# Kernel tuning notes

Hardware: AMD Instinct MI355X
Metric: run time of the kernel (lower is better)

The kernel has to match this reference:

```python
import jax, jax.numpy as jnp
import numpy as np

B, N, IN, OUT = 16, 1000, 128, 128


def setup_inputs() -> dict:
    key = jax.random.key(0)
    ks = jax.random.split(key, 8)
    stdv = 1.0 / np.sqrt(IN + OUT)  # matches reset_param uniform(-stdv, stdv)
    def w(k):
        return jax.random.uniform(k, (N, IN + OUT, OUT), jnp.float32, -stdv, stdv)
    return {
        "xt": jax.random.normal(ks[0], (B, N, IN), jnp.float32),
        "hidden": jax.random.normal(ks[1], (1, N, OUT), jnp.float32),
        "ct_1": jax.random.normal(ks[2], (1, N, OUT), jnp.float32),
        "W_i": w(ks[3]), "b_i": jnp.zeros((N, OUT), jnp.float32),
        "W_o": w(ks[4]), "b_o": jnp.zeros((N, OUT), jnp.float32),
        "W_f": w(ks[5]), "b_f": jnp.zeros((N, OUT), jnp.float32),
        "W_c": w(ks[6]), "b_c": jnp.zeros((N, OUT), jnp.float32),
    }


def reference(xt, hidden, ct_1, W_i, b_i, W_o, b_o, W_f, b_f, W_c, b_c):
    b = xt.shape[0]
    h = jnp.broadcast_to(hidden, (b,) + hidden.shape[1:])       # [B,N,OUT]
    xh = jnp.concatenate([xt, h], axis=-1)                      # [B,N,IN+OUT]

    def gate(W, bias, act):
        # per-stock batched matmul: [B,N,K] x [N,K,O] -> [B,N,O]
        return act(jnp.einsum('bnk,nko->bno', xh, W) + bias)

    it = gate(W_i, b_i, jax.nn.sigmoid)
    ot = gate(W_o, b_o, jax.nn.sigmoid)
    ft = gate(W_f, b_f, jax.nn.sigmoid)
    chat = gate(W_c, b_c, jnp.tanh)

    ct = ft * jnp.broadcast_to(ct_1, it.shape) + it * chat
    ht = ot * jnp.tanh(ct)
    return ht, ct
```

## Files before the change

kernel.cpp:

```cpp
#include <hip/hip_runtime.h>
#include <hip/hip_bf16.h>

namespace {
constexpr int B   = 16;
constexpr int NS  = 1000;
constexpr int IN  = 128;
constexpr int OUT = 128;
constexpr int K   = 256;

typedef __attribute__((ext_vector_type(8))) short short8;
typedef __attribute__((ext_vector_type(4))) float f32x4;

__device__ __forceinline__ float fsigmoid(float x) {
  return 1.0f / (1.0f + __expf(-x));
}
__device__ __forceinline__ float ftanh(float x) {
  return 2.0f / (1.0f + __expf(-2.0f * x)) - 1.0f;
}
__device__ __forceinline__ unsigned int f2bf(float f) {
  unsigned int u = __builtin_bit_cast(unsigned int, f);
  u += 0x7fffu + ((u >> 16) & 1u);
  return u >> 16;
}
__device__ __forceinline__ unsigned int pack2(float lo, float hi) {
  return f2bf(lo) | (f2bf(hi) << 16);
}

__global__ __launch_bounds__(512, 2) void lstm_kernel(
    const float* __restrict__ xt, const float* __restrict__ hidden,
    const float* __restrict__ ct_1,
    const float* __restrict__ Wi, const float* __restrict__ bi,
    const float* __restrict__ Wo, const float* __restrict__ bo,
    const float* __restrict__ Wf, const float* __restrict__ bfp,
    const float* __restrict__ Wc, const float* __restrict__ bc,
    float* __restrict__ out) {
  __shared__ __align__(16) unsigned char smem[40960];

  const int n   = blockIdx.x;
  const int tid = threadIdx.x;

  {
    const int b  = tid >> 5;
    const int s  = tid & 31;
    const int k0 = s << 3;
    float v[8];
    if (k0 < IN) {
      const float4 a = *reinterpret_cast<const float4*>(xt + ((size_t)b * NS + n) * IN + k0);
      const float4 c = *reinterpret_cast<const float4*>(xt + ((size_t)b * NS + n) * IN + k0 + 4);
      v[0]=a.x; v[1]=a.y; v[2]=a.z; v[3]=a.w; v[4]=c.x; v[5]=c.y; v[6]=c.z; v[7]=c.w;
    } else {
      const float4 a = *reinterpret_cast<const float4*>(hidden + (size_t)n * OUT + (k0 - IN));
      const float4 c = *reinterpret_cast<const float4*>(hidden + (size_t)n * OUT + (k0 - IN) + 4);
      v[0]=a.x; v[1]=a.y; v[2]=a.z; v[3]=a.w; v[4]=c.x; v[5]=c.y; v[6]=c.z; v[7]=c.w;
    }
    uint4 pk;
    pk.x = pack2(v[0], v[1]); pk.y = pack2(v[2], v[3]);
    pk.z = pack2(v[4], v[5]); pk.w = pack2(v[6], v[7]);
    const int addr = ((b << 9) + (s << 4)) ^ ((b & 7) << 4);
    *reinterpret_cast<uint4*>(&smem[addr]) = pk;
  }
  __syncthreads();

  const int wid  = tid >> 6;
  const int g    = wid >> 1;
  const int half = wid & 1;
  const int l    = tid & 63;
  const int g2   = l >> 4;
  const int c16  = l & 15;

  const float* Wg = (g == 0) ? Wi : (g == 1) ? Wo : (g == 2) ? Wf : Wc;
  const float* bg = (g == 0) ? bi : (g == 1) ? bo : (g == 2) ? bfp : bc;
  const float* wgp = Wg + (size_t)n * (K * OUT) + half * 64 + l;

  const int wsl = 8192 + (wid << 12);
  f32x4 acc[4] = {f32x4{0,0,0,0}, f32x4{0,0,0,0}, f32x4{0,0,0,0}, f32x4{0,0,0,0}};

  #pragma unroll
  for (int c = 0; c < 8; ++c) {
    float wr[8][4];
    #pragma unroll
    for (int i = 0; i < 8; ++i)
      #pragma unroll
      for (int j = 0; j < 4; ++j)
        wr[i][j] = wgp[(size_t)((c << 5) + (i << 2) + j) * OUT];
    #pragma unroll
    for (int i = 0; i < 8; ++i) {
      uint2 pw;
      pw.x = pack2(wr[i][0], wr[i][1]);
      pw.y = pack2(wr[i][2], wr[i][3]);
      const int a = (wsl + (l << 6) + (i << 3)) ^ ((l & 7) << 4);
      *reinterpret_cast<uint2*>(&smem[a]) = pw;
    }
    const int aaddr = ((c16 << 9) + (c << 6) + (g2 << 4)) ^ ((c16 & 7) << 4);
    const short8 af = *reinterpret_cast<const short8*>(&smem[aaddr]);
    #pragma unroll
    for (int t = 0; t < 4; ++t) {
      const int col   = (t << 4) + c16;
      const int baddr = (wsl + (col << 6) + (g2 << 4)) ^ ((col & 7) << 4);
      const short8 bf = *reinterpret_cast<const short8*>(&smem[baddr]);
      acc[t] = __builtin_amdgcn_mfma_f32_16x16x32_bf16(af, bf, acc[t], 0, 0, 0);
    }
  }

  __syncthreads();
  float* gb = reinterpret_cast<float*>(&smem[8192]);
  #pragma unroll
  for (int t = 0; t < 4; ++t) {
    const int colg = (half << 6) + (t << 4) + c16;
    const float bias = bg[(size_t)n * OUT + colg];
    #pragma unroll
    for (int r = 0; r < 4; ++r) {
      const int b = (g2 << 2) + r;
      gb[g * 2048 + b * 128 + colg] = acc[t][r] + bias;
    }
  }
  __syncthreads();

  const size_t nbase = (size_t)n * OUT;
  #pragma unroll
  for (int r = 0; r < 4; ++r) {
    const int p = tid + (r << 9);
    const int b = p >> 7;
    const int o = p & 127;
    const float gi = gb[0 * 2048 + b * 128 + o];
    const float go = gb[1 * 2048 + b * 128 + o];
    const float gf = gb[2 * 2048 + b * 128 + o];
    const float gc = gb[3 * 2048 + b * 128 + o];
    const float it = fsigmoid(gi);
    const float ot = fsigmoid(go);
    const float ft = fsigmoid(gf);
    const float ch = ftanh(gc);
    const float cp = ct_1[nbase + o];
    const float ct = ft * cp + it * ch;
    const float ht = ot * ftanh(ct);
    const size_t oidx = (size_t)b * ((size_t)NS * OUT) + nbase + o;
    out[oidx] = ht;
    out[(size_t)B * NS * OUT + oidx] = ct;
  }
}
}

extern "C" void kernel_launch(void* const* d_in, const int* in_sizes, int n_in,
                              void* d_out, int out_size, void* d_ws, size_t ws_size,
                              hipStream_t stream) {
  const float* xt     = (const float*)d_in[0];
  const float* hidden = (const float*)d_in[1];
  const float* ct_1   = (const float*)d_in[2];
  const float* Wi     = (const float*)d_in[3];
  const float* bi     = (const float*)d_in[4];
  const float* Wo     = (const float*)d_in[5];
  const float* bo     = (const float*)d_in[6];
  const float* Wf     = (const float*)d_in[7];
  const float* bf     = (const float*)d_in[8];
  const float* Wc     = (const float*)d_in[9];
  const float* bc     = (const float*)d_in[10];

  lstm_kernel<<<NS, 512, 0, stream>>>(xt, hidden, ct_1, Wi, bi, Wo, bo,
                                      Wf, bf, Wc, bc,
                                      (float*)d_out);
}
```

Baseline: 114.8 us.

## Vectorize weight loads, double-buffer them in registers, and pad gate buffer

Weight loads change from scalar strided reads to float4 vector loads over four adjacent output columns. Two register buffers prefetch the next K-chunk while the current one is packed to bf16 and fed to MFMA, overlapping global latency with compute. The shared-memory slice layout is reorganised with a new swizzle to suit the transposed packing, and the gate staging buffer gets row padding to reduce bank conflicts. This raises register pressure and risks lower occupancy.

Measured after the change: 110.6 us. 1.04x faster.

```diff
diff --git a/kernel.cpp b/kernel.cpp
--- a/kernel.cpp
+++ b/kernel.cpp
@@ -24,6 +24,9 @@
 }
 __device__ __forceinline__ unsigned int pack2(float lo, float hi) {
   return f2bf(lo) | (f2bf(hi) << 16);
+}
+__device__ __forceinline__ int slice_addr(int base, int kq, int col) {
+  return base + (kq << 10) + ((col << 4) ^ (((col >> 3) & 7) << 4));
 }
 
 __global__ __launch_bounds__(512, 2) void lstm_kernel(
@@ -70,40 +73,79 @@
 
   const float* Wg = (g == 0) ? Wi : (g == 1) ? Wo : (g == 2) ? Wf : Wc;
   const float* bg = (g == 0) ? bi : (g == 1) ? bo : (g == 2) ? bfp : bc;
-  const float* wgp = Wg + (size_t)n * (K * OUT) + half * 64 + l;
+  const float* wbase = Wg + (size_t)n * (K * OUT) + half * 64 + (c16 << 2);
 
   const int wsl = 8192 + (wid << 12);
   f32x4 acc[4] = {f32x4{0,0,0,0}, f32x4{0,0,0,0}, f32x4{0,0,0,0}, f32x4{0,0,0,0}};
 
-  #pragma unroll
-  for (int c = 0; c < 8; ++c) {
-    float wr[8][4];
-    #pragma unroll
-    for (int i = 0; i < 8; ++i)
+  float4 wqa[8], wqb[8];
+  #pragma unroll
+  for (int i = 0; i < 8; ++i)
+    wqa[i] = *reinterpret_cast<const float4*>(wbase + (size_t)((g2 << 3) + i) * OUT);
+  #pragma unroll
+  for (int i = 0; i < 8; ++i)
+    wqb[i] = *reinterpret_cast<const float4*>(wbase + (size_t)(32 + (g2 << 3) + i) * OUT);
+
+  #pragma unroll 1
+  for (int c = 0; c < 8; c += 2) {
+    {
+      uint4 pk[4];
+      #pragma unroll
+      for (int j = 0; j < 4; ++j) {
+        pk[j].x = pack2((&wqa[0].x)[j], (&wqa[1].x)[j]);
+        pk[j].y = pack2((&wqa[2].x)[j], (&wqa[3].x)[j]);
+        pk[j].z = pack2((&wqa[4].x)[j], (&wqa[5].x)[j]);
+        pk[j].w = pack2((&wqa[6].x)[j], (&wqa[7].x)[j]);
+      }
+      const int cn = (c + 2 < 8) ? c + 2 : 0;
+      #pragma unroll
+      for (int i = 0; i < 8; ++i)
+        wqa[i] = *reinterpret_cast<const float4*>(
+            wbase + (size_t)((cn << 5) + (g2 << 3) + i) * OUT);
       #pragma unroll
       for (int j = 0; j < 4; ++j)
-        wr[i][j] = wgp[(size_t)((c << 5) + (i << 2) + j) * OUT];
-    #pragma unroll
-    for (int i = 0; i < 8; ++i) {
-      uint2 pw;
-      pw.x = pack2(wr[i][0], wr[i][1]);
-      pw.y = pack2(wr[i][2], wr[i][3]);
-      const int a = (wsl + (l << 6) + (i << 3)) ^ ((l & 7) << 4);
-      *reinterpret_cast<uint2*>(&smem[a]) = pw;
-    }
-    const int aaddr = ((c16 << 9) + (c << 6) + (g2 << 4)) ^ ((c16 & 7) << 4);
-    const short8 af = *reinterpret_cast<const short8*>(&smem[aaddr]);
-    #pragma unroll
-    for (int t = 0; t < 4; ++t) {
-      const int col   = (t << 4) + c16;
-      const int baddr = (wsl + (col << 6) + (g2 << 4)) ^ ((col & 7) << 4);
-      const short8 bf = *reinterpret_cast<const short8*>(&smem[baddr]);
-      acc[t] = __builtin_amdgcn_mfma_f32_16x16x32_bf16(af, bf, acc[t], 0, 0, 0);
+        *reinterpret_cast<uint4*>(&smem[slice_addr(wsl, g2, (c16 << 2) + j)]) = pk[j];
+
+      const int aaddr = ((c16 << 9) + (c << 6) + (g2 << 4)) ^ ((c16 & 7) << 4);
+      const short8 af = *reinterpret_cast<const short8*>(&smem[aaddr]);
+      #pragma unroll
+      for (int t = 0; t < 4; ++t) {
+        const short8 bfv = *reinterpret_cast<const short8*>(
+            &smem[slice_addr(wsl, g2, (t << 4) + c16)]);
+        acc[t] = __builtin_amdgcn_mfma_f32_16x16x32_bf16(af, bfv, acc[t], 0, 0, 0);
+      }
+    }
+    {
+      uint4 pk[4];
+      #pragma unroll
+      for (int j = 0; j < 4; ++j) {
+        pk[j].x = pack2((&wqb[0].x)[j], (&wqb[1].x)[j]);
+        pk[j].y = pack2((&wqb[2].x)[j], (&wqb[3].x)[j]);
+        pk[j].z = pack2((&wqb[4].x)[j], (&wqb[5].x)[j]);
+        pk[j].w = pack2((&wqb[6].x)[j], (&wqb[7].x)[j]);
+      }
+      const int cn = (c + 3 < 8) ? c + 3 : 0;
+      #pragma unroll
+      for (int i = 0; i < 8; ++i)
+        wqb[i] = *reinterpret_cast<const float4*>(
+            wbase + (size_t)((cn << 5) + (g2 << 3) + i) * OUT);
+      #pragma unroll
+      for (int j = 0; j < 4; ++j)
+        *reinterpret_cast<uint4*>(&smem[slice_addr(wsl, g2, (c16 << 2) + j)]) = pk[j];
+
+      const int aaddr = ((c16 << 9) + ((c + 1) << 6) + (g2 << 4)) ^ ((c16 & 7) << 4);
+      const short8 af = *reinterpret_cast<const short8*>(&smem[aaddr]);
+      #pragma unroll
+      for (int t = 0; t < 4; ++t) {
+        const short8 bfv = *reinterpret_cast<const short8*>(
+            &smem[slice_addr(wsl, g2, (t << 4) + c16)]);
+        acc[t] = __builtin_amdgcn_mfma_f32_16x16x32_bf16(af, bfv, acc[t], 0, 0, 0);
+      }
     }
   }
 
   __syncthreads();
-  float* gb = reinterpret_cast<float*>(&smem[8192]);
+  float* gb = reinterpret_cast<float*>(smem);
   #pragma unroll
   for (int t = 0; t < 4; ++t) {
     const int colg = (half << 6) + (t << 4) + c16;
@@ -111,7 +153,7 @@
     #pragma unroll
     for (int r = 0; r < 4; ++r) {
       const int b = (g2 << 2) + r;
-      gb[g * 2048 + b * 128 + colg] = acc[t][r] + bias;
+      gb[g * 2064 + b * 129 + colg] = acc[t][r] + bias;
     }
   }
   __syncthreads();
@@ -122,10 +164,10 @@
     const int p = tid + (r << 9);
     const int b = p >> 7;
     const int o = p & 127;
-    const float gi = gb[0 * 2048 + b * 128 + o];
-    const float go = gb[1 * 2048 + b * 128 + o];
-    const float gf = gb[2 * 2048 + b * 128 + o];
-    const float gc = gb[3 * 2048 + b * 128 + o];
+    const float gi = gb[0 * 2064 + b * 129 + o];
+    const float go = gb[1 * 2064 + b * 129 + o];
+    const float gf = gb[2 * 2064 + b * 129 + o];
+    const float gc = gb[3 * 2064 + b * 129 + o];
     const float it = fsigmoid(gi);
     const float ot = fsigmoid(go);
     const float ft = fsigmoid(gf);
```

## Load weights directly into MFMA B-fragment registers, skipping LDS staging

Applied to the files above, without the earlier changes.

Each lane now loads the eight K-consecutive weight values it needs for the MFMA B operand straight from global memory, packs them to bf16 in registers, and feeds the MFMA. This removes the per-chunk LDS write/read round-trip of the weight tile. LDS shrinks, the gate buffer is padded (stride 129) to avoid bank conflicts, and launch bounds request higher occupancy with the loop no longer unrolled. The trade-off is that each global load now covers only 16 contiguous floats per row, giving less coalescing, and less unrolling means less memory-level parallelism per wave.

Result: faster. 109.6 us (-4.5%).

```diff
diff --git a/kernel.cpp b/kernel.cpp
--- a/kernel.cpp
+++ b/kernel.cpp
@@ -26,7 +26,7 @@
   return f2bf(lo) | (f2bf(hi) << 16);
 }
 
-__global__ __launch_bounds__(512, 2) void lstm_kernel(
+__global__ __launch_bounds__(512, 6) void lstm_kernel(
     const float* __restrict__ xt, const float* __restrict__ hidden,
     const float* __restrict__ ct_1,
     const float* __restrict__ Wi, const float* __restrict__ bi,
@@ -34,7 +34,7 @@
     const float* __restrict__ Wf, const float* __restrict__ bfp,
     const float* __restrict__ Wc, const float* __restrict__ bc,
     float* __restrict__ out) {
-  __shared__ __align__(16) unsigned char smem[40960];
+  __shared__ __align__(16) unsigned char smem[33024];
 
   const int n   = blockIdx.x;
   const int tid = threadIdx.x;
@@ -70,40 +70,37 @@
 
   const float* Wg = (g == 0) ? Wi : (g == 1) ? Wo : (g == 2) ? Wf : Wc;
   const float* bg = (g == 0) ? bi : (g == 1) ? bo : (g == 2) ? bfp : bc;
-  const float* wgp = Wg + (size_t)n * (K * OUT) + half * 64 + l;
+  const float* wq = Wg + (size_t)n * (K * OUT) + (size_t)(g2 << 3) * OUT + half * 64 + c16;
 
-  const int wsl = 8192 + (wid << 12);
   f32x4 acc[4] = {f32x4{0,0,0,0}, f32x4{0,0,0,0}, f32x4{0,0,0,0}, f32x4{0,0,0,0}};
 
-  #pragma unroll
+  #pragma unroll 1
   for (int c = 0; c < 8; ++c) {
-    float wr[8][4];
+    float w[4][8];
     #pragma unroll
-    for (int i = 0; i < 8; ++i)
+    for (int t = 0; t < 4; ++t)
       #pragma unroll
-      for (int j = 0; j < 4; ++j)
-        wr[i][j] = wgp[(size_t)((c << 5) + (i << 2) + j) * OUT];
-    #pragma unroll
-    for (int i = 0; i < 8; ++i) {
-      uint2 pw;
-      pw.x = pack2(wr[i][0], wr[i][1]);
-      pw.y = pack2(wr[i][2], wr[i][3]);
-      const int a = (wsl + (l << 6) + (i << 3)) ^ ((l & 7) << 4);
-      *reinterpret_cast<uint2*>(&smem[a]) = pw;
-    }
+      for (int j = 0; j < 8; ++j)
+        w[t][j] = wq[(j << 7) + (t << 4)];
+    wq += 32 * OUT;
+
     const int aaddr = ((c16 << 9) + (c << 6) + (g2 << 4)) ^ ((c16 & 7) << 4);
     const short8 af = *reinterpret_cast<const short8*>(&smem[aaddr]);
+
     #pragma unroll
     for (int t = 0; t < 4; ++t) {
-      const int col   = (t << 4) + c16;
-      const int baddr = (wsl + (col << 6) + (g2 << 4)) ^ ((col & 7) << 4);
-      const short8 bf = *reinterpret_cast<const short8*>(&smem[baddr]);
-      acc[t] = __builtin_amdgcn_mfma_f32_16x16x32_bf16(af, bf, acc[t], 0, 0, 0);
+      uint4 bu;
+      bu.x = pack2(w[t][0], w[t][1]);
+      bu.y = pack2(w[t][2], w[t][3]);
+      bu.z = pack2(w[t][4], w[t][5]);
+      bu.w = pack2(w[t][6], w[t][7]);
+      const short8 bfv = __builtin_bit_cast(short8, bu);
+      acc[t] = __builtin_amdgcn_mfma_f32_16x16x32_bf16(af, bfv, acc[t], 0, 0, 0);
     }
   }
 
   __syncthreads();
-  float* gb = reinterpret_cast<float*>(&smem[8192]);
+  float* gb = reinterpret_cast<float*>(smem);
   #pragma unroll
   for (int t = 0; t < 4; ++t) {
     const int colg = (half << 6) + (t << 4) + c16;
@@ -111,7 +108,7 @@
     #pragma unroll
     for (int r = 0; r < 4; ++r) {
       const int b = (g2 << 2) + r;
-      gb[g * 2048 + b * 128 + colg] = acc[t][r] + bias;
+      gb[g * 2064 + b * 129 + colg] = acc[t][r] + bias;
     }
   }
   __syncthreads();
@@ -122,10 +119,10 @@
     const int p = tid + (r << 9);
     const int b = p >> 7;
     const int o = p & 127;
-    const float gi = gb[0 * 2048 + b * 128 + o];
-    const float go = gb[1 * 2048 + b * 128 + o];
-    const float gf = gb[2 * 2048 + b * 128 + o];
-    const float gc = gb[3 * 2048 + b * 128 + o];
+    const float gi = gb[0 * 2064 + b * 129 + o];
+    const float go = gb[1 * 2064 + b * 129 + o];
+    const float gf = gb[2 * 2064 + b * 129 + o];
+    const float gc = gb[3 * 2064 + b * 129 + o];
     const float it = fsigmoid(gi);
     const float ot = fsigmoid(go);
     const float ft = fsigmoid(gf);
```
